# Optimization experiments

Measured on AMD Instinct MI355X. Metric: run time of the kernel, lower is better.

## Reference

```python
import jax, jax.numpy as jnp
import numpy as np

B, S, E, H = 16, 2048, 512, 64


def setup_inputs() -> dict:
    key = jax.random.key(0)
    k1, k2, k3, k4, k5 = jax.random.split(key, 5)
    inp = {
        "input": jax.random.normal(k1, (B, S, E), dtype=jnp.float32),
        "seq_lengths": jax.random.randint(k2, (B,), 0, S).astype(jnp.int64),
        "Wq": jax.random.normal(k3, (E, H), dtype=jnp.float32) * (1.0 / np.sqrt(E)),
        "Wk": jax.random.normal(k4, (E, H), dtype=jnp.float32) * (1.0 / np.sqrt(E)),
        "Wv": jax.random.normal(k5, (E, H), dtype=jnp.float32) * (1.0 / np.sqrt(E)),
    }
    return inp


def reference(input, seq_lengths, Wq, Wk, Wv):
    # Projections (bias-free Linear): [B,S,E] @ [E,H] -> [B,S,H]
    q = input @ Wq
    k = input @ Wk
    v = input @ Wv
    Sdim = input.shape[1]
    head_size = Wk.shape[-1]
    # Padding mask: position >= seq_length -> True. Zero out q and k (NOT v),
    # exactly as the torch module does with masked_fill.
    pad = (jnp.arange(Sdim)[None, :] >= seq_lengths[:, None])[:, :, None]  # [B,S,1]
    q = jnp.where(pad, 0.0, q)
    k = jnp.where(pad, 0.0, k)
    scale = 1.0 / np.sqrt(head_size).astype(np.float32)
    # Full score matrix [B,S,S] (the memory-bound intermediate)
    scores = jnp.einsum("bsh,bth->bst", q, k) * scale
    weights = jax.nn.softmax(scores, axis=-1)
    weights = jnp.where(jnp.isnan(weights), 0.0, weights)
    out = jnp.einsum("bst,bth->bsh", weights, v)  # [B,S,H]
    return out
```

## Files before the change

kernel.cpp:

```cpp
#include <hip/hip_runtime.h>
#include <hip/hip_bf16.h>

typedef __bf16 bf16;
typedef __bf16 bf16x8 __attribute__((ext_vector_type(8)));
typedef __bf16 bf16x4 __attribute__((ext_vector_type(4)));
typedef float  f32x4  __attribute__((ext_vector_type(4)));
typedef float  f32x16 __attribute__((ext_vector_type(16)));
typedef unsigned int u32x4 __attribute__((ext_vector_type(4)));

static constexpr int SDIM = 2048;
static constexpr int EDIM = 512;
static constexpr int HDIM = 64;

typedef __attribute__((address_space(1))) const void* gptr_t;
typedef __attribute__((address_space(3))) void*       lptr_t;

__device__ __forceinline__ void gl_lds16(const bf16* g, bf16* l) {
  __builtin_amdgcn_global_load_lds((gptr_t)g, (lptr_t)l, 16, 0, 0);
}

#if __has_builtin(__builtin_amdgcn_exp2f)
#define EXP2F(x) __builtin_amdgcn_exp2f(x)
#else
#define EXP2F(x) exp2f(x)
#endif

__device__ __forceinline__ bf16x8 pack8(f32x4 a, f32x4 b) {
  bf16x8 r;
  r[0] = (bf16)a[0]; r[1] = (bf16)a[1]; r[2] = (bf16)a[2]; r[3] = (bf16)a[3];
  r[4] = (bf16)b[0]; r[5] = (bf16)b[1]; r[6] = (bf16)b[2]; r[7] = (bf16)b[3];
  return r;
}

__device__ __forceinline__ unsigned cvtpk_bf16(float a, float b) {
  unsigned r;
  asm("v_cvt_pk_bf16_f32 %0, %1, %2" : "=v"(r) : "v"(a), "v"(b));
  return r;
}

__global__ __launch_bounds__(256) void wt_kernel(const float* __restrict__ Wq,
                                                 const float* __restrict__ Wk,
                                                 const float* __restrict__ Wv,
                                                 bf16* __restrict__ Wt) {
  __shared__ float lds[64][65];
  const int mat = blockIdx.x >> 3;
  const int et  = blockIdx.x & 7;
  const float* W = (mat == 0) ? Wq : ((mat == 1) ? Wk : Wv);
  const float scale = (mat == 0) ? 0.18033688f : 1.0f;
  const int t  = threadIdx.x;
  const int er = t >> 2;
  const int c4 = (t & 3) * 16;
#pragma unroll
  for (int j = 0; j < 4; ++j) {
    f32x4 v = *(const f32x4*)(W + (size_t)(et * 64 + er) * HDIM + c4 + j * 4);
    lds[er][c4 + j * 4 + 0] = v[0]; lds[er][c4 + j * 4 + 1] = v[1];
    lds[er][c4 + j * 4 + 2] = v[2]; lds[er][c4 + j * 4 + 3] = v[3];
  }
  __syncthreads();
  const int h  = t >> 2;
  const int ec = (t & 3) * 16;
  bf16x8 o0, o1;
#pragma unroll
  for (int j = 0; j < 8; ++j) o0[j] = (bf16)(lds[ec + j][h] * scale);
#pragma unroll
  for (int j = 0; j < 8; ++j) o1[j] = (bf16)(lds[ec + 8 + j][h] * scale);
  bf16* dst = Wt + mat * (HDIM * EDIM) + (size_t)h * EDIM + et * 64 + ec;
  *(bf16x8*)dst = o0;
  *(bf16x8*)(dst + 8) = o1;
}

__global__ __launch_bounds__(256) void proj_kernel(const float* __restrict__ x,
                                                   const bf16* __restrict__ Wt,
                                                   const int* __restrict__ lens,
                                                   bf16* __restrict__ qo,
                                                   bf16* __restrict__ ko,
                                                   bf16* __restrict__ vT) {
  __shared__ __align__(16) bf16 wbuf[2][192 * 64];
  const int tid  = threadIdx.x;
  const int wave = tid >> 6;
  const int lane = tid & 63;
  const int quad = lane >> 4;
  const int l16  = lane & 15;
  const int rowbase = blockIdx.x * 64 + wave * 16;
  const int b = blockIdx.x >> 5;
  const float* xrow = x + (size_t)(rowbase + l16) * EDIM + quad * 8;
  const int srow   = lane >> 3;
  const int schunk = (lane & 7) ^ srow;

  #define WSTAGE(ck, buf) { _Pragma("unroll")                                  \
    for (int i6 = 0; i6 < 6; ++i6) {                                           \
      const int R0 = (wave * 6 + i6) * 8;                                      \
      gl_lds16(Wt + (size_t)(R0 + srow) * EDIM + (ck) * 64 + schunk * 8,       \
               &(buf)[R0 * 64]); } }

  f32x4 acc[3][4];
#pragma unroll
  for (int m = 0; m < 3; ++m)
#pragma unroll
    for (int nt = 0; nt < 4; ++nt) acc[m][nt] = (f32x4){0.f, 0.f, 0.f, 0.f};

  #define WCOMPUTE(buf, eo4, afrag) { _Pragma("unroll")                        \
    for (int m = 0; m < 3; ++m) { _Pragma("unroll")                            \
      for (int nt = 0; nt < 4; ++nt) {                                         \
        bf16x8 bfv = *(const bf16x8*)(&(buf)[(m * 64 + nt * 16 + l16) * 64 +   \
                                             ((((eo4) + quad) ^ (l16 & 7)) * 8)]); \
        acc[m][nt] = __builtin_amdgcn_mfma_f32_16x16x32_bf16(afrag, bfv, acc[m][nt], 0, 0, 0); } } }

  WSTAGE(0, wbuf[0]);
  __builtin_amdgcn_sched_barrier(0);
  f32x4 c0 = *(const f32x4*)(xrow);
  f32x4 c1 = *(const f32x4*)(xrow + 4);
  f32x4 c2 = *(const f32x4*)(xrow + 32);
  f32x4 c3 = *(const f32x4*)(xrow + 36);
  f32x4 n0 = *(const f32x4*)(xrow + 64);
  f32x4 n1 = *(const f32x4*)(xrow + 68);
  f32x4 n2 = *(const f32x4*)(xrow + 96);
  f32x4 n3 = *(const f32x4*)(xrow + 100);
  __builtin_amdgcn_sched_barrier(0);
  asm volatile("s_waitcnt vmcnt(8)" ::: "memory");
  __builtin_amdgcn_s_barrier();
  __builtin_amdgcn_sched_barrier(0);

#pragma unroll
  for (int ck = 0; ck < 8; ++ck) {
    const int cs = (ck < 7) ? (ck + 1) : 7;
    WSTAGE(cs, wbuf[(ck + 1) & 1]);
    __builtin_amdgcn_sched_barrier(0);
    const int kf = (ck < 6) ? (ck + 2) : 7;
    f32x4 m0 = *(const f32x4*)(xrow + kf * 64);
    f32x4 m1 = *(const f32x4*)(xrow + kf * 64 + 4);
    f32x4 m2 = *(const f32x4*)(xrow + kf * 64 + 32);
    f32x4 m3 = *(const f32x4*)(xrow + kf * 64 + 36);
    __builtin_amdgcn_sched_barrier(0);
    bf16x8 a = pack8(c0, c1);
    WCOMPUTE(wbuf[ck & 1], 0, a);
    a = pack8(c2, c3);
    WCOMPUTE(wbuf[ck & 1], 4, a);
    c0 = n0; c1 = n1; c2 = n2; c3 = n3;
    n0 = m0; n1 = m1; n2 = m2; n3 = m3;
    asm volatile("s_waitcnt vmcnt(4)" ::: "memory");
    __builtin_amdgcn_s_barrier();
    __builtin_amdgcn_sched_barrier(0);
  }

  int odd_or = 0;
#pragma unroll
  for (int i = 1; i < 16; i += 2) odd_or |= lens[i];
  const int len = (odd_or == 0) ? lens[2 * b] : lens[b];

#pragma unroll
  for (int nt = 0; nt < 4; ++nt) {
    const int h = nt * 16 + l16;
    bf16x4 vv;
#pragma unroll
    for (int r = 0; r < 4; ++r) {
      const int row = rowbase + quad * 4 + r;
      const int s = row & (SDIM - 1);
      const bool pad = (s >= len);
      qo[(size_t)row * HDIM + h] = (bf16)(pad ? 0.f : acc[0][nt][r]);
      ko[(size_t)row * HDIM + h] = (bf16)(pad ? 0.f : acc[1][nt][r]);
      vv[r] = (bf16)acc[2][nt][r];
    }
    *(bf16x4*)(vT + ((size_t)b * HDIM + h) * SDIM + (rowbase & (SDIM - 1)) + quad * 4) = vv;
  }
  #undef WSTAGE
  #undef WCOMPUTE
}

__global__ __launch_bounds__(256) void attn_kernel(const bf16* __restrict__ qb,
                                                   const bf16* __restrict__ kb,
                                                   const bf16* __restrict__ vT,
                                                   float* __restrict__ out) {
  __shared__ __align__(16) bf16 Kbuf[2][2][64 * 64];
  __shared__ __align__(16) bf16 Vbuf[2][2][64 * 64];
  const int tid  = threadIdx.x;
  const int wave = tid >> 6;
  const int lane = tid & 63;
  const int hi   = lane >> 5;
  const int l32  = lane & 31;
  const int iq   = wave & 1;
  const int jk   = wave >> 1;
  const int xcd = blockIdx.x & 7;
  const int jj  = blockIdx.x >> 3;
  const int b   = xcd * 2 + (jj >> 5);
  const int qbase = (jj & 31) * 64 + iq * 32;
  const bf16* q0 = qb + (size_t)b * SDIM * HDIM;
  const bf16* k0 = kb + (size_t)b * SDIM * HDIM;
  const bf16* v0 = vT + (size_t)b * HDIM * SDIM;
  const int srow   = lane >> 3;
  const int schunk = (lane & 7) ^ srow;
  const int rswz   = (l32 & 7) << 4;

  bf16x8 qf[4];
#pragma unroll
  for (int c = 0; c < 4; ++c)
    qf[c] = *(const bf16x8*)(q0 + (size_t)(qbase + l32) * HDIM + c * 16 + hi * 8);

  f32x16 O[2];
#pragma unroll
  for (int ht = 0; ht < 2; ++ht)
#pragma unroll
    for (int r = 0; r < 16; ++r) O[ht][r] = 0.f;
  float l_acc = 0.f;

  #define STAGE(sidx, db) {                                                    \
    const int key0_ = (wave & 1) * 1024 + (sidx) * 64;                         \
    if (wave < 2) {                                                            \
      const bf16* gk = k0 + (size_t)(key0_ + srow) * HDIM + schunk * 8;        \
      bf16* lk = &Kbuf[db][wave & 1][0];                                       \
      _Pragma("unroll")                                                        \
      for (int r8 = 0; r8 < 8; ++r8)                                           \
        gl_lds16(gk + (size_t)r8 * 8 * HDIM, lk + r8 * 8 * 64);                \
    } else {                                                                   \
      const bf16* gv = v0 + (size_t)srow * SDIM + key0_ + schunk * 8;          \
      bf16* lv = &Vbuf[db][wave & 1][0];                                       \
      _Pragma("unroll")                                                        \
      for (int r8 = 0; r8 < 8; ++r8)                                           \
        gl_lds16(gv + (size_t)r8 * 8 * SDIM, lv + r8 * 8 * 64);                \
    }                                                                          \
  }

  STAGE(0, 0);
#pragma unroll 2
  for (int s = 0; s < 16; ++s) {
    __syncthreads();
    if (s + 1 < 16) STAGE(s + 1, (s + 1) & 1);
    const bf16* KB = &Kbuf[s & 1][jk][0];
    const bf16* VB = &Vbuf[s & 1][jk][0];

    bf16x8 pa[4];
#pragma unroll
    for (int kt = 0; kt < 2; ++kt) {
      f32x16 st;
#pragma unroll
      for (int r = 0; r < 16; ++r) st[r] = 0.f;
      const int krow = kt * 32 + l32;
#pragma unroll
      for (int c = 0; c < 4; ++c) {
        bf16x8 kf = *(const bf16x8*)((const char*)KB + krow * 128 +
                                     ((c * 32 + hi * 16) ^ rswz));
        st = __builtin_amdgcn_mfma_f32_32x32x16_bf16(kf, qf[c], st, 0, 0, 0);
      }
      float p[16];
#pragma unroll
      for (int r = 0; r < 16; ++r) p[r] = EXP2F(st[r]);
      float s0 = (p[0] + p[1]) + (p[2] + p[3]);
      float s1 = (p[4] + p[5]) + (p[6] + p[7]);
      float s2 = (p[8] + p[9]) + (p[10] + p[11]);
      float s3 = (p[12] + p[13]) + (p[14] + p[15]);
      l_acc += (s0 + s1) + (s2 + s3);
      unsigned u0 = cvtpk_bf16(p[0], p[1]);
      unsigned u1 = cvtpk_bf16(p[2], p[3]);
      unsigned u2 = cvtpk_bf16(p[4], p[5]);
      unsigned u3 = cvtpk_bf16(p[6], p[7]);
      asm("v_permlane32_swap_b32 %0, %1" : "+v"(u0), "+v"(u2));
      asm("v_permlane32_swap_b32 %0, %1" : "+v"(u1), "+v"(u3));
      union { u32x4 u; bf16x8 v; } f0;
      f0.u[0] = u0; f0.u[1] = u1; f0.u[2] = u2; f0.u[3] = u3;
      pa[kt * 2 + 0] = f0.v;
      unsigned u4 = cvtpk_bf16(p[8],  p[9]);
      unsigned u5 = cvtpk_bf16(p[10], p[11]);
      unsigned u6 = cvtpk_bf16(p[12], p[13]);
      unsigned u7 = cvtpk_bf16(p[14], p[15]);
      asm("v_permlane32_swap_b32 %0, %1" : "+v"(u4), "+v"(u6));
      asm("v_permlane32_swap_b32 %0, %1" : "+v"(u5), "+v"(u7));
      union { u32x4 u; bf16x8 v; } f1;
      f1.u[0] = u4; f1.u[1] = u5; f1.u[2] = u6; f1.u[3] = u7;
      pa[kt * 2 + 1] = f1.v;
    }
#pragma unroll
    for (int ht = 0; ht < 2; ++ht) {
      const int vrow = ht * 32 + l32;
#pragma unroll
      for (int tc = 0; tc < 4; ++tc) {
        bf16x8 vf = *(const bf16x8*)((const char*)VB + vrow * 128 +
                                     ((tc * 32 + hi * 16) ^ rswz));
        O[ht] = __builtin_amdgcn_mfma_f32_32x32x16_bf16(pa[tc], vf, O[ht], 0, 0, 0);
      }
    }
  }

  l_acc += __shfl_xor(l_acc, 32);

  float* cb = (float*)&Kbuf[0][0][0];
  float* cl = (float*)&Vbuf[0][0][0];
  __syncthreads();
  if (jk == 1) {
#pragma unroll
    for (int ht = 0; ht < 2; ++ht)
#pragma unroll
      for (int r = 0; r < 16; ++r) {
        const int qrow = (r & 3) + 8 * (r >> 2) + 4 * hi;
        cb[(iq * 32 + qrow) * 64 + ht * 32 + l32] = O[ht][r];
      }
    if (hi == 0) cl[iq * 32 + l32] = l_acc;
  }
  __syncthreads();
  if (jk == 0) {
    const float inv_own = 1.0f / (l_acc + cl[iq * 32 + l32]);
#pragma unroll
    for (int r = 0; r < 16; ++r) {
      const int qrow = (r & 3) + 8 * (r >> 2) + 4 * hi;
      const float inv = __shfl(inv_own, qrow);
#pragma unroll
      for (int ht = 0; ht < 2; ++ht) {
        const float val = (O[ht][r] + cb[(iq * 32 + qrow) * 64 + ht * 32 + l32]) * inv;
        out[((size_t)b * SDIM + qbase + qrow) * HDIM + ht * 32 + l32] = val;
      }
    }
  }
  #undef STAGE
}

extern "C" void kernel_launch(void* const* d_in, const int* in_sizes, int n_in,
                              void* d_out, int out_size, void* d_ws, size_t ws_size,
                              hipStream_t stream) {
  (void)in_sizes; (void)n_in; (void)out_size; (void)ws_size;
  const float* x  = (const float*)d_in[0];
  const int*   sl = (const int*)d_in[1];
  const float* Wq = (const float*)d_in[2];
  const float* Wk = (const float*)d_in[3];
  const float* Wv = (const float*)d_in[4];
  float* out = (float*)d_out;

  char* ws = (char*)d_ws;
  bf16* Wt = (bf16*)(ws);
  bf16* qb = (bf16*)(ws + (256 << 10));
  bf16* kb = (bf16*)(ws + (256 << 10) + (4 << 20));
  bf16* vT = (bf16*)(ws + (256 << 10) + (8 << 20));

  wt_kernel  <<<24,  256, 0, stream>>>(Wq, Wk, Wv, Wt);
  proj_kernel<<<512, 256, 0, stream>>>(x, Wt, sl, qb, kb, vT);
  attn_kernel<<<512, 256, 0, stream>>>(qb, kb, vT, out);
}
```

Baseline: 135.9 us.

## Repartition attention waves so each wave covers all 64 queries over a 32-key slice

```diff
diff --git a/kernel.cpp b/kernel.cpp
--- a/kernel.cpp
+++ b/kernel.cpp
@@ -167,23 +167,24 @@
   #undef WCOMPUTE
 }
 
-__global__ __launch_bounds__(256) void attn_kernel(const bf16* __restrict__ qb,
-                                                   const bf16* __restrict__ kb,
-                                                   const bf16* __restrict__ vT,
-                                                   float* __restrict__ out) {
+__global__ __launch_bounds__(256, 2) void attn_kernel(const bf16* __restrict__ qb,
+                                                      const bf16* __restrict__ kb,
+                                                      const bf16* __restrict__ vT,
+                                                      float* __restrict__ out) {
   __shared__ __align__(16) bf16 Kbuf[2][2][64 * 64];
   __shared__ __align__(16) bf16 Vbuf[2][2][64 * 64];
+  __shared__ float Lsh[256];
   const int tid  = threadIdx.x;
   const int wave = tid >> 6;
   const int lane = tid & 63;
   const int hi   = lane >> 5;
   const int l32  = lane & 31;
-  const int iq   = wave & 1;
-  const int jk   = wave >> 1;
+  const int half = wave >> 1;
+  const int sub  = wave & 1;
   const int xcd = blockIdx.x & 7;
   const int jj  = blockIdx.x >> 3;
   const int b   = xcd * 2 + (jj >> 5);
-  const int qbase = (jj & 31) * 64 + iq * 32;
+  const int qbase = (jj & 31) * 64;
   const bf16* q0 = qb + (size_t)b * SDIM * HDIM;
   const bf16* k0 = kb + (size_t)b * SDIM * HDIM;
   const bf16* v0 = vT + (size_t)b * HDIM * SDIM;
@@ -191,17 +192,18 @@
   const int schunk = (lane & 7) ^ srow;
   const int rswz   = (l32 & 7) << 4;
 
-  bf16x8 qf[4];
-#pragma unroll
-  for (int c = 0; c < 4; ++c)
-    qf[c] = *(const bf16x8*)(q0 + (size_t)(qbase + l32) * HDIM + c * 16 + hi * 8);
-
-  f32x16 O[2];
-#pragma unroll
-  for (int ht = 0; ht < 2; ++ht)
-#pragma unroll
-    for (int r = 0; r < 16; ++r) O[ht][r] = 0.f;
-  float l_acc = 0.f;
+  bf16x8 qf[2][4];
+#pragma unroll
+  for (int qh = 0; qh < 2; ++qh)
+#pragma unroll
+    for (int c = 0; c < 4; ++c)
+      qf[qh][c] = *(const bf16x8*)(q0 + (size_t)(qbase + qh * 32 + l32) * HDIM +
+                                   c * 16 + hi * 8);
+
+  f32x16 O00, O01, O10, O11;
+#pragma unroll
+  for (int r = 0; r < 16; ++r) { O00[r] = 0.f; O01[r] = 0.f; O10[r] = 0.f; O11[r] = 0.f; }
+  float l0 = 0.f, l1 = 0.f;
 
   #define STAGE(sidx, db) {                                                    \
     const int key0_ = (wave & 1) * 1024 + (sidx) * 64;                         \
@@ -225,22 +227,34 @@
   for (int s = 0; s < 16; ++s) {
     __syncthreads();
     if (s + 1 < 16) STAGE(s + 1, (s + 1) & 1);
-    const bf16* KB = &Kbuf[s & 1][jk][0];
-    const bf16* VB = &Vbuf[s & 1][jk][0];
-
-    bf16x8 pa[4];
-#pragma unroll
-    for (int kt = 0; kt < 2; ++kt) {
+    const bf16* KB = &Kbuf[s & 1][half][0];
+    const bf16* VB = &Vbuf[s & 1][half][0];
+
+    bf16x8 kf[4];
+    const int krow = sub * 32 + l32;
+#pragma unroll
+    for (int c = 0; c < 4; ++c)
+      kf[c] = *(const bf16x8*)((const char*)KB + krow * 128 +
+                               ((c * 32 + hi * 16) ^ rswz));
+    bf16x8 vf[2][2];
+#pragma unroll
+    for (int ht = 0; ht < 2; ++ht)
+#pragma unroll
+      for (int tc = 0; tc < 2; ++tc)
+        vf[ht][tc] = *(const bf16x8*)((const char*)VB + (ht * 32 + l32) * 128 +
+                                      ((sub * 64 + tc * 32 + hi * 16) ^ rswz));
+
+    bf16x8 pa[2][2];
+#pragma unroll
+    for (int qh = 0; qh < 2; ++qh) {
       f32x16 st;
 #pragma unroll
       for (int r = 0; r < 16; ++r) st[r] = 0.f;
-      const int krow = kt * 32 + l32;
-#pragma unroll
-      for (int c = 0; c < 4; ++c) {
-        bf16x8 kf = *(const bf16x8*)((const char*)KB + krow * 128 +
-                                     ((c * 32 + hi * 16) ^ rswz));
-        st = __builtin_amdgcn_mfma_f32_32x32x16_bf16(kf, qf[c], st, 0, 0, 0);
-      }
+      __builtin_amdgcn_s_setprio(1);
+#pragma unroll
+      for (int c = 0; c < 4; ++c)
+        st = __builtin_amdgcn_mfma_f32_32x32x16_bf16(kf[c], qf[qh][c], st, 0, 0, 0);
+      __builtin_amdgcn_s_setprio(0);
       float p[16];
 #pragma unroll
       for (int r = 0; r < 16; ++r) p[r] = EXP2F(st[r]);
@@ -248,7 +262,7 @@
       float s1 = (p[4] + p[5]) + (p[6] + p[7]);
       float s2 = (p[8] + p[9]) + (p[10] + p[11]);
       float s3 = (p[12] + p[13]) + (p[14] + p[15]);
-      l_acc += (s0 + s1) + (s2 + s3);
+      if (qh == 0) l0 += (s0 + s1) + (s2 + s3); else l1 += (s0 + s1) + (s2 + s3);
       unsigned u0 = cvtpk_bf16(p[0], p[1]);
       unsigned u1 = cvtpk_bf16(p[2], p[3]);
       unsigned u2 = cvtpk_bf16(p[4], p[5]);
@@ -257,7 +271,7 @@
       asm("v_permlane32_swap_b32 %0, %1" : "+v"(u1), "+v"(u3));
       union { u32x4 u; bf16x8 v; } f0;
       f0.u[0] = u0; f0.u[1] = u1; f0.u[2] = u2; f0.u[3] = u3;
-      pa[kt * 2 + 0] = f0.v;
+      pa[qh][0] = f0.v;
       unsigned u4 = cvtpk_bf16(p[8],  p[9]);
       unsigned u5 = cvtpk_bf16(p[10], p[11]);
       unsigned u6 = cvtpk_bf16(p[12], p[13]);
@@ -266,47 +280,53 @@
       asm("v_permlane32_swap_b32 %0, %1" : "+v"(u5), "+v"(u7));
       union { u32x4 u; bf16x8 v; } f1;
       f1.u[0] = u4; f1.u[1] = u5; f1.u[2] = u6; f1.u[3] = u7;
-      pa[kt * 2 + 1] = f1.v;
-    }
-#pragma unroll
-    for (int ht = 0; ht < 2; ++ht) {
-      const int vrow = ht * 32 + l32;
-#pragma unroll
-      for (int tc = 0; tc < 4; ++tc) {
-        bf16x8 vf = *(const bf16x8*)((const char*)VB + vrow * 128 +
-                                     ((tc * 32 + hi * 16) ^ rswz));
-        O[ht] = __builtin_amdgcn_mfma_f32_32x32x16_bf16(pa[tc], vf, O[ht], 0, 0, 0);
-      }
-    }
-  }
-
-  l_acc += __shfl_xor(l_acc, 32);
-
-  float* cb = (float*)&Kbuf[0][0][0];
-  float* cl = (float*)&Vbuf[0][0][0];
+      pa[qh][1] = f1.v;
+    }
+    __builtin_amdgcn_s_setprio(1);
+#pragma unroll
+    for (int tc = 0; tc < 2; ++tc) {
+      O00 = __builtin_amdgcn_mfma_f32_32x32x16_bf16(pa[0][tc], vf[0][tc], O00, 0, 0, 0);
+      O01 = __builtin_amdgcn_mfma_f32_32x32x16_bf16(pa[0][tc], vf[1][tc], O01, 0, 0, 0);
+      O10 = __builtin_amdgcn_mfma_f32_32x32x16_bf16(pa[1][tc], vf[0][tc], O10, 0, 0, 0);
+      O11 = __builtin_amdgcn_mfma_f32_32x32x16_bf16(pa[1][tc], vf[1][tc], O11, 0, 0, 0);
+    }
+    __builtin_amdgcn_s_setprio(0);
+  }
+
+  l0 += __shfl_xor(l0, 32);
+  l1 += __shfl_xor(l1, 32);
+
   __syncthreads();
-  if (jk == 1) {
-#pragma unroll
-    for (int ht = 0; ht < 2; ++ht)
-#pragma unroll
-      for (int r = 0; r < 16; ++r) {
-        const int qrow = (r & 3) + 8 * (r >> 2) + 4 * hi;
-        cb[(iq * 32 + qrow) * 64 + ht * 32 + l32] = O[ht][r];
-      }
-    if (hi == 0) cl[iq * 32 + l32] = l_acc;
-  }
-  __syncthreads();
-  if (jk == 0) {
-    const float inv_own = 1.0f / (l_acc + cl[iq * 32 + l32]);
+  {
+    float* pb = (wave < 2) ? ((float*)&Kbuf[0][0][0] + wave * 4096)
+                           : ((float*)&Vbuf[0][0][0] + (wave - 2) * 4096);
 #pragma unroll
     for (int r = 0; r < 16; ++r) {
       const int qrow = (r & 3) + 8 * (r >> 2) + 4 * hi;
-      const float inv = __shfl(inv_own, qrow);
-#pragma unroll
-      for (int ht = 0; ht < 2; ++ht) {
-        const float val = (O[ht][r] + cb[(iq * 32 + qrow) * 64 + ht * 32 + l32]) * inv;
-        out[((size_t)b * SDIM + qbase + qrow) * HDIM + ht * 32 + l32] = val;
-      }
+      pb[0 * 1024 + qrow * 32 + l32] = O00[r];
+      pb[1 * 1024 + qrow * 32 + l32] = O01[r];
+      pb[2 * 1024 + qrow * 32 + l32] = O10[r];
+      pb[3 * 1024 + qrow * 32 + l32] = O11[r];
+    }
+    if (hi == 0) {
+      Lsh[wave * 64 + l32]      = l0;
+      Lsh[wave * 64 + 32 + l32] = l1;
+    }
+  }
+  __syncthreads();
+  {
+    const float* K0 = (const float*)&Kbuf[0][0][0];
+    const float* V0 = (const float*)&Vbuf[0][0][0];
+    const int qh  = wave >> 1;
+    const int jr0 = (wave & 1) * 16;
+#pragma unroll
+    for (int j = 0; j < 16; ++j) {
+      const int qrow = jr0 + j;
+      const int idx  = (qh * 2 + hi) * 1024 + qrow * 32 + l32;
+      const float v = (K0[idx] + K0[4096 + idx]) + (V0[idx] + V0[4096 + idx]);
+      const int qq = qh * 32 + qrow;
+      const float lt = (Lsh[qq] + Lsh[64 + qq]) + (Lsh[128 + qq] + Lsh[192 + qq]);
+      out[((size_t)b * SDIM + qbase + qq) * HDIM + hi * 32 + l32] = v * (1.0f / lt);
     }
   }
   #undef STAGE
```

New measurement: 137.8 us. About the same (+1.4%).

## Skip padded key windows in attention using precomputed padded-V column sums

Applied to the files above, without the earlier changes.

```diff
diff --git a/kernel.cpp b/kernel.cpp
--- a/kernel.cpp
+++ b/kernel.cpp
@@ -41,7 +41,13 @@
 __global__ __launch_bounds__(256) void wt_kernel(const float* __restrict__ Wq,
                                                  const float* __restrict__ Wk,
                                                  const float* __restrict__ Wv,
-                                                 bf16* __restrict__ Wt) {
+                                                 bf16* __restrict__ Wt,
+                                                 float* __restrict__ vpad) {
+  if (blockIdx.x >= 24) {
+#pragma unroll
+    for (int i = 0; i < 4; ++i) vpad[threadIdx.x + i * 256] = 0.f;
+    return;
+  }
   __shared__ float lds[64][65];
   const int mat = blockIdx.x >> 3;
   const int et  = blockIdx.x & 7;
@@ -74,7 +80,8 @@
                                                    const int* __restrict__ lens,
                                                    bf16* __restrict__ qo,
                                                    bf16* __restrict__ ko,
-                                                   bf16* __restrict__ vT) {
+                                                   bf16* __restrict__ vT,
+                                                   float* __restrict__ vpad) {
   __shared__ __align__(16) bf16 wbuf[2][192 * 64];
   const int tid  = threadIdx.x;
   const int wave = tid >> 6;
@@ -163,6 +170,17 @@
     }
     *(bf16x4*)(vT + ((size_t)b * HDIM + h) * SDIM + (rowbase & (SDIM - 1)) + quad * 4) = vv;
   }
+
+  const int s0 = (blockIdx.x & 31) * 64;
+  if (s0 >= len) {
+#pragma unroll
+    for (int nt = 0; nt < 4; ++nt) {
+      float sum = (acc[2][nt][0] + acc[2][nt][1]) + (acc[2][nt][2] + acc[2][nt][3]);
+      sum += __shfl_xor(sum, 16);
+      sum += __shfl_xor(sum, 32);
+      if (quad == 0) atomicAdd(&vpad[b * 64 + nt * 16 + l16], sum);
+    }
+  }
   #undef WSTAGE
   #undef WCOMPUTE
 }
@@ -170,6 +188,8 @@
 __global__ __launch_bounds__(256) void attn_kernel(const bf16* __restrict__ qb,
                                                    const bf16* __restrict__ kb,
                                                    const bf16* __restrict__ vT,
+                                                   const int* __restrict__ lens,
+                                                   const float* __restrict__ vpad,
                                                    float* __restrict__ out) {
   __shared__ __align__(16) bf16 Kbuf[2][2][64 * 64];
   __shared__ __align__(16) bf16 Vbuf[2][2][64 * 64];
@@ -180,10 +200,8 @@
   const int l32  = lane & 31;
   const int iq   = wave & 1;
   const int jk   = wave >> 1;
-  const int xcd = blockIdx.x & 7;
-  const int jj  = blockIdx.x >> 3;
-  const int b   = xcd * 2 + (jj >> 5);
-  const int qbase = (jj & 31) * 64 + iq * 32;
+  const int b    = blockIdx.x >> 5;
+  const int qbase = (blockIdx.x & 31) * 64 + iq * 32;
   const bf16* q0 = qb + (size_t)b * SDIM * HDIM;
   const bf16* k0 = kb + (size_t)b * SDIM * HDIM;
   const bf16* v0 = vT + (size_t)b * HDIM * SDIM;
@@ -191,6 +209,13 @@
   const int schunk = (lane & 7) ^ srow;
   const int rswz   = (l32 & 7) << 4;
 
+  int odd_or = 0;
+#pragma unroll
+  for (int i = 1; i < 16; i += 2) odd_or |= lens[i];
+  const int len = (odd_or == 0) ? lens[2 * b] : lens[b];
+  const int W    = (len + 63) >> 6;
+  const int Smax = (W + 1) >> 1;
+
   bf16x8 qf[4];
 #pragma unroll
   for (int c = 0; c < 4; ++c)
@@ -203,8 +228,8 @@
     for (int r = 0; r < 16; ++r) O[ht][r] = 0.f;
   float l_acc = 0.f;
 
-  #define STAGE(sidx, db) {                                                    \
-    const int key0_ = (wave & 1) * 1024 + (sidx) * 64;                         \
+  #define STAGE(wnd, db) {                                                     \
+    const int key0_ = (wnd) * 64;                                              \
     if (wave < 2) {                                                            \
       const bf16* gk = k0 + (size_t)(key0_ + srow) * HDIM + schunk * 8;        \
       bf16* lk = &Kbuf[db][wave & 1][0];                                       \
@@ -220,67 +245,79 @@
     }                                                                          \
   }
 
-  STAGE(0, 0);
-#pragma unroll 2
-  for (int s = 0; s < 16; ++s) {
-    __syncthreads();
-    if (s + 1 < 16) STAGE(s + 1, (s + 1) & 1);
-    const bf16* KB = &Kbuf[s & 1][jk][0];
-    const bf16* VB = &Vbuf[s & 1][jk][0];
-
-    bf16x8 pa[4];
-#pragma unroll
-    for (int kt = 0; kt < 2; ++kt) {
-      f32x16 st;
-#pragma unroll
-      for (int r = 0; r < 16; ++r) st[r] = 0.f;
-      const int krow = kt * 32 + l32;
-#pragma unroll
-      for (int c = 0; c < 4; ++c) {
-        bf16x8 kf = *(const bf16x8*)((const char*)KB + krow * 128 +
-                                     ((c * 32 + hi * 16) ^ rswz));
-        st = __builtin_amdgcn_mfma_f32_32x32x16_bf16(kf, qf[c], st, 0, 0, 0);
-      }
-      float p[16];
-#pragma unroll
-      for (int r = 0; r < 16; ++r) p[r] = EXP2F(st[r]);
-      float s0 = (p[0] + p[1]) + (p[2] + p[3]);
-      float s1 = (p[4] + p[5]) + (p[6] + p[7]);
-      float s2 = (p[8] + p[9]) + (p[10] + p[11]);
-      float s3 = (p[12] + p[13]) + (p[14] + p[15]);
-      l_acc += (s0 + s1) + (s2 + s3);
-      unsigned u0 = cvtpk_bf16(p[0], p[1]);
-      unsigned u1 = cvtpk_bf16(p[2], p[3]);
-      unsigned u2 = cvtpk_bf16(p[4], p[5]);
-      unsigned u3 = cvtpk_bf16(p[6], p[7]);
-      asm("v_permlane32_swap_b32 %0, %1" : "+v"(u0), "+v"(u2));
-      asm("v_permlane32_swap_b32 %0, %1" : "+v"(u1), "+v"(u3));
-      union { u32x4 u; bf16x8 v; } f0;
-      f0.u[0] = u0; f0.u[1] = u1; f0.u[2] = u2; f0.u[3] = u3;
-      pa[kt * 2 + 0] = f0.v;
-      unsigned u4 = cvtpk_bf16(p[8],  p[9]);
-      unsigned u5 = cvtpk_bf16(p[10], p[11]);
-      unsigned u6 = cvtpk_bf16(p[12], p[13]);
-      unsigned u7 = cvtpk_bf16(p[14], p[15]);
-      asm("v_permlane32_swap_b32 %0, %1" : "+v"(u4), "+v"(u6));
-      asm("v_permlane32_swap_b32 %0, %1" : "+v"(u5), "+v"(u7));
-      union { u32x4 u; bf16x8 v; } f1;
-      f1.u[0] = u4; f1.u[1] = u5; f1.u[2] = u6; f1.u[3] = u7;
-      pa[kt * 2 + 1] = f1.v;
+  if (W > 0) {
+    { const int w0 = ((wave & 1) < W) ? (wave & 1) : (W - 1); STAGE(w0, 0); }
+    for (int s = 0; s < Smax; ++s) {
+      __syncthreads();
+      if (s + 1 < Smax) {
+        int wn = 2 * (s + 1) + (wave & 1);
+        if (wn > W - 1) wn = W - 1;
+        STAGE(wn, (s + 1) & 1);
+      }
+      const int myw = 2 * s + jk;
+      if (myw < W) {
+        const bf16* KB = &Kbuf[s & 1][jk][0];
+        const bf16* VB = &Vbuf[s & 1][jk][0];
+
+        bf16x8 pa[4];
+#pragma unroll
+        for (int kt = 0; kt < 2; ++kt) {
+          f32x16 st;
+#pragma unroll
+          for (int r = 0; r < 16; ++r) st[r] = 0.f;
+          const int krow = kt * 32 + l32;
+#pragma unroll
+          for (int c = 0; c < 4; ++c) {
+            bf16x8 kf = *(const bf16x8*)((const char*)KB + krow * 128 +
+                                         ((c * 32 + hi * 16) ^ rswz));
+            st = __builtin_amdgcn_mfma_f32_32x32x16_bf16(kf, qf[c], st, 0, 0, 0);
+          }
+          float p[16];
+#pragma unroll
+          for (int r = 0; r < 16; ++r) p[r] = EXP2F(st[r]);
+          float s0 = (p[0] + p[1]) + (p[2] + p[3]);
+          float s1 = (p[4] + p[5]) + (p[6] + p[7]);
+          float s2 = (p[8] + p[9]) + (p[10] + p[11]);
+          float s3 = (p[12] + p[13]) + (p[14] + p[15]);
+          l_acc += (s0 + s1) + (s2 + s3);
+          unsigned u0 = cvtpk_bf16(p[0], p[1]);
+          unsigned u1 = cvtpk_bf16(p[2], p[3]);
+          unsigned u2 = cvtpk_bf16(p[4], p[5]);
+          unsigned u3 = cvtpk_bf16(p[6], p[7]);
+          asm("v_permlane32_swap_b32 %0, %1" : "+v"(u0), "+v"(u2));
+          asm("v_permlane32_swap_b32 %0, %1" : "+v"(u1), "+v"(u3));
+          union { u32x4 u; bf16x8 v; } f0;
+          f0.u[0] = u0; f0.u[1] = u1; f0.u[2] = u2; f0.u[3] = u3;
+          pa[kt * 2 + 0] = f0.v;
+          unsigned u4 = cvtpk_bf16(p[8],  p[9]);
+          unsigned u5 = cvtpk_bf16(p[10], p[11]);
+          unsigned u6 = cvtpk_bf16(p[12], p[13]);
+          unsigned u7 = cvtpk_bf16(p[14], p[15]);
+          asm("v_permlane32_swap_b32 %0, %1" : "+v"(u4), "+v"(u6));
+          asm("v_permlane32_swap_b32 %0, %1" : "+v"(u5), "+v"(u7));
+          union { u32x4 u; bf16x8 v; } f1;
+          f1.u[0] = u4; f1.u[1] = u5; f1.u[2] = u6; f1.u[3] = u7;
+          pa[kt * 2 + 1] = f1.v;
+        }
+#pragma unroll
+        for (int ht = 0; ht < 2; ++ht) {
+          const int vrow = ht * 32 + l32;
+#pragma unroll
+          for (int tc = 0; tc < 4; ++tc) {
+            bf16x8 vf = *(const bf16x8*)((const char*)VB + vrow * 128 +
+                                         ((tc * 32 + hi * 16) ^ rswz));
+            O[ht] = __builtin_amdgcn_mfma_f32_32x32x16_bf16(pa[tc], vf, O[ht], 0, 0, 0);
+          }
+        }
+      }
     }
-#pragma unroll
-    for (int ht = 0; ht < 2; ++ht) {
-      const int vrow = ht * 32 + l32;
-#pragma unroll
-      for (int tc = 0; tc < 4; ++tc) {
-        bf16x8 vf = *(const bf16x8*)((const char*)VB + vrow * 128 +
-                                     ((tc * 32 + hi * 16) ^ rswz));
-        O[ht] = __builtin_amdgcn_mfma_f32_32x32x16_bf16(pa[tc], vf, O[ht], 0, 0, 0);
-      }
-    }
   }
 
   l_acc += __shfl_xor(l_acc, 32);
+
+  const float vp0 = vpad[b * 64 + 0 * 32 + l32];
+  const float vp1 = vpad[b * 64 + 1 * 32 + l32];
+  const float padl = (float)(SDIM - W * 64);
 
   float* cb = (float*)&Kbuf[0][0][0];
   float* cl = (float*)&Vbuf[0][0][0];
@@ -297,15 +334,18 @@
   }
   __syncthreads();
   if (jk == 0) {
-    const float inv_own = 1.0f / (l_acc + cl[iq * 32 + l32]);
+    const float inv_own = 1.0f / (l_acc + cl[iq * 32 + l32] + padl);
 #pragma unroll
     for (int r = 0; r < 16; ++r) {
       const int qrow = (r & 3) + 8 * (r >> 2) + 4 * hi;
       const float inv = __shfl(inv_own, qrow);
-#pragma unroll
-      for (int ht = 0; ht < 2; ++ht) {
-        const float val = (O[ht][r] + cb[(iq * 32 + qrow) * 64 + ht * 32 + l32]) * inv;
-        out[((size_t)b * SDIM + qbase + qrow) * HDIM + ht * 32 + l32] = val;
+      {
+        const float val = (O[0][r] + cb[(iq * 32 + qrow) * 64 + 0 * 32 + l32] + vp0) * inv;
+        out[((size_t)b * SDIM + qbase + qrow) * HDIM + 0 * 32 + l32] = val;
+      }
+      {
+        const float val = (O[1][r] + cb[(iq * 32 + qrow) * 64 + 1 * 32 + l32] + vp1) * inv;
+        out[((size_t)b * SDIM + qbase + qrow) * HDIM + 1 * 32 + l32] = val;
       }
     }
   }
@@ -324,12 +364,13 @@
   float* out = (float*)d_out;
 
   char* ws = (char*)d_ws;
-  bf16* Wt = (bf16*)(ws);
-  bf16* qb = (bf16*)(ws + (256 << 10));
-  bf16* kb = (bf16*)(ws + (256 << 10) + (4 << 20));
-  bf16* vT = (bf16*)(ws + (256 << 10) + (8 << 20));
-
-  wt_kernel  <<<24,  256, 0, stream>>>(Wq, Wk, Wv, Wt);
-  proj_kernel<<<512, 256, 0, stream>>>(x, Wt, sl, qb, kb, vT);
-  attn_kernel<<<512, 256, 0, stream>>>(qb, kb, vT, out);
-}
+  bf16*  Wt   = (bf16*)(ws);
+  float* vpad = (float*)(ws + (192 << 10));
+  bf16*  qb   = (bf16*)(ws + (256 << 10));
+  bf16*  kb   = (bf16*)(ws + (256 << 10) + (4 << 20));
+  bf16*  vT   = (bf16*)(ws + (256 << 10) + (8 << 20));
+
+  wt_kernel  <<<25,  256, 0, stream>>>(Wq, Wk, Wv, Wt, vpad);
+  proj_kernel<<<512, 256, 0, stream>>>(x, Wt, sl, qb, kb, vT, vpad);
+  attn_kernel<<<512, 256, 0, stream>>>(qb, kb, vT, sl, vpad, out);
+}
```

Result: slower. 139.4 us (+2.6%).

## Software-pipeline PV MFMAs one tile behind QK and softmax

Applied to the files above, without the earlier changes.

```diff
diff --git a/kernel.cpp b/kernel.cpp
--- a/kernel.cpp
+++ b/kernel.cpp
@@ -203,6 +203,9 @@
     for (int r = 0; r < 16; ++r) O[ht][r] = 0.f;
   float l_acc = 0.f;
 
+  bf16x8 paP[4];
+  bf16x8 vfP[2][4];
+
   #define STAGE(sidx, db) {                                                    \
     const int key0_ = (wave & 1) * 1024 + (sidx) * 64;                         \
     if (wave < 2) {                                                            \
@@ -228,19 +231,31 @@
     const bf16* KB = &Kbuf[s & 1][jk][0];
     const bf16* VB = &Vbuf[s & 1][jk][0];
 
-    bf16x8 pa[4];
+    bf16x8 kf[2][4];
+#pragma unroll
+    for (int kt = 0; kt < 2; ++kt)
+#pragma unroll
+      for (int c = 0; c < 4; ++c)
+        kf[kt][c] = *(const bf16x8*)((const char*)KB + (kt * 32 + l32) * 128 +
+                                     ((c * 32 + hi * 16) ^ rswz));
+
+    if (s) {
+#pragma unroll
+      for (int ht = 0; ht < 2; ++ht)
+#pragma unroll
+        for (int tc = 0; tc < 4; ++tc)
+          O[ht] = __builtin_amdgcn_mfma_f32_32x32x16_bf16(paP[tc], vfP[ht][tc], O[ht], 0, 0, 0);
+    }
+
+    bf16x8 paC[4];
 #pragma unroll
     for (int kt = 0; kt < 2; ++kt) {
       f32x16 st;
 #pragma unroll
       for (int r = 0; r < 16; ++r) st[r] = 0.f;
-      const int krow = kt * 32 + l32;
-#pragma unroll
-      for (int c = 0; c < 4; ++c) {
-        bf16x8 kf = *(const bf16x8*)((const char*)KB + krow * 128 +
-                                     ((c * 32 + hi * 16) ^ rswz));
-        st = __builtin_amdgcn_mfma_f32_32x32x16_bf16(kf, qf[c], st, 0, 0, 0);
-      }
+#pragma unroll
+      for (int c = 0; c < 4; ++c)
+        st = __builtin_amdgcn_mfma_f32_32x32x16_bf16(kf[kt][c], qf[c], st, 0, 0, 0);
       float p[16];
 #pragma unroll
       for (int r = 0; r < 16; ++r) p[r] = EXP2F(st[r]);
@@ -257,7 +272,7 @@
       asm("v_permlane32_swap_b32 %0, %1" : "+v"(u1), "+v"(u3));
       union { u32x4 u; bf16x8 v; } f0;
       f0.u[0] = u0; f0.u[1] = u1; f0.u[2] = u2; f0.u[3] = u3;
-      pa[kt * 2 + 0] = f0.v;
+      paC[kt * 2 + 0] = f0.v;
       unsigned u4 = cvtpk_bf16(p[8],  p[9]);
       unsigned u5 = cvtpk_bf16(p[10], p[11]);
       unsigned u6 = cvtpk_bf16(p[12], p[13]);
@@ -266,19 +281,24 @@
       asm("v_permlane32_swap_b32 %0, %1" : "+v"(u5), "+v"(u7));
       union { u32x4 u; bf16x8 v; } f1;
       f1.u[0] = u4; f1.u[1] = u5; f1.u[2] = u6; f1.u[3] = u7;
-      pa[kt * 2 + 1] = f1.v;
+      paC[kt * 2 + 1] = f1.v;
     }
-#pragma unroll
-    for (int ht = 0; ht < 2; ++ht) {
-      const int vrow = ht * 32 + l32;
-#pragma unroll
-      for (int tc = 0; tc < 4; ++tc) {
-        bf16x8 vf = *(const bf16x8*)((const char*)VB + vrow * 128 +
-                                     ((tc * 32 + hi * 16) ^ rswz));
-        O[ht] = __builtin_amdgcn_mfma_f32_32x32x16_bf16(pa[tc], vf, O[ht], 0, 0, 0);
-      }
-    }
-  }
+
+#pragma unroll
+    for (int ht = 0; ht < 2; ++ht)
+#pragma unroll
+      for (int tc = 0; tc < 4; ++tc)
+        vfP[ht][tc] = *(const bf16x8*)((const char*)VB + (ht * 32 + l32) * 128 +
+                                       ((tc * 32 + hi * 16) ^ rswz));
+#pragma unroll
+    for (int i = 0; i < 4; ++i) paP[i] = paC[i];
+  }
+
+#pragma unroll
+  for (int ht = 0; ht < 2; ++ht)
+#pragma unroll
+    for (int tc = 0; tc < 4; ++tc)
+      O[ht] = __builtin_amdgcn_mfma_f32_32x32x16_bf16(paP[tc], vfP[ht][tc], O[ht], 0, 0, 0);
 
   l_acc += __shfl_xor(l_acc, 32);
 
```

Measured after the change: 136.6 us. No clear change (+0.6%).
